# Optimization experiments

Hardware: AMD Instinct MI355X
Metric: run time of the kernel (lower is better)

## Reference

```python
import jax, jax.numpy as jnp
import numpy as np

LATENT_NUM = 64
N_FEATURES = 10000
BATCH = 4096


def setup_inputs() -> dict:
    key = jax.random.key(0)
    k1, k2 = jax.random.split(key)
    inputs = jax.random.normal(k1, (BATCH, N_FEATURES), dtype=jnp.float32)
    # TruncatedNormal(mean=0, stddev=0.01) approximated with clipped normal
    embedding = jnp.clip(
        jax.random.normal(k2, (N_FEATURES, LATENT_NUM), dtype=jnp.float32) * 0.01,
        -0.02, 0.02,
    )
    return {"inputs": inputs, "embedding": embedding}


def reference(inputs, embedding):
    # Original TF code, per latent dim f:
    #   ex2 = (sum over batch AND features of V[:,f]*X)^2   (reduce_sum w/o axis)
    # Vectorized: t[f] = sum_b (X @ V)[b,f];  q[f] = sum_{b} (X^2 @ V^2)[b,f]
    xv = inputs @ embedding                      # [B, F]
    t = jnp.sum(xv, axis=0)                      # [F]
    q = jnp.sum((inputs * inputs) @ (embedding * embedding), axis=(0, 1))  # scalar
    return 0.5 * (jnp.sum(t * t) - q)
```

## Files before the change

### kernel.cpp

```cpp
#include <hip/hip_runtime.h>

#define NROWS 4096
#define NCOLS 10000
#define NLAT  64
#define NCOLG 2500
#define TPB   256
#define NBX   10
#define NRC   128
#define RPC   32
#define NCB   40
#define CPB   250
#define NSLICE 16
#define CPS   (NRC / NSLICE)
#define NBLK2 (NCB * NSLICE)

__global__ __launch_bounds__(TPB) void colsum_partials(
        const float* __restrict__ X,
        float* __restrict__ ps, float* __restrict__ ps2) {
    int jg = blockIdx.x * TPB + threadIdx.x;
    if (jg >= NCOLG) return;
    const float* p = X + (size_t)blockIdx.y * RPC * NCOLS + (size_t)jg * 4;
    float s0=0.f,s1=0.f,s2=0.f,s3=0.f,q0=0.f,q1=0.f,q2=0.f,q3=0.f;
    #pragma unroll 8
    for (int r = 0; r < RPC; ++r) {
        float4 v = *reinterpret_cast<const float4*>(p);
        p += NCOLS;
        s0 += v.x; s1 += v.y; s2 += v.z; s3 += v.w;
        q0 = fmaf(v.x, v.x, q0); q1 = fmaf(v.y, v.y, q1);
        q2 = fmaf(v.z, v.z, q2); q3 = fmaf(v.w, v.w, q3);
    }
    size_t o = (size_t)blockIdx.y * NCOLS + (size_t)jg * 4;
    *reinterpret_cast<float4*>(ps  + o) = make_float4(s0, s1, s2, s3);
    *reinterpret_cast<float4*>(ps2 + o) = make_float4(q0, q1, q2, q3);
}

__global__ __launch_bounds__(TPB) void fold_qt(
        const float* __restrict__ ps, const float* __restrict__ ps2,
        const float* __restrict__ V, float* __restrict__ tpT) {
    const int cb = blockIdx.x;
    const int sl = blockIdx.y;
    const int tid = threadIdx.x;
    __shared__ float lds_s[CPB], lds_s2[CPB];
    if (tid < CPB) {
        const int col = cb * CPB + tid;
        float s = 0.f, s2 = 0.f;
        const int c0 = sl * CPS;
        #pragma unroll
        for (int c = c0; c < c0 + CPS; ++c) {
            s  += ps [(size_t)c * NCOLS + col];
            s2 += ps2[(size_t)c * NCOLS + col];
        }
        lds_s[tid] = s; lds_s2[tid] = s2;
    }
    __syncthreads();

    const int lane = tid & 63, w = tid >> 6;
    float at = 0.f, aq = 0.f;
    const float* Vb = V + (size_t)cb * CPB * NLAT;
    #pragma unroll 4
    for (int c = w; c < CPB; c += 4) {
        float v = Vb[(size_t)c * NLAT + lane];
        at = fmaf(lds_s[c], v, at);
        aq = fmaf(lds_s2[c], v * v, aq);
    }
    #pragma unroll
    for (int st = 1; st < 64; st <<= 1) aq += __shfl_xor(aq, st, 64);

    __shared__ float lt[4][NLAT];
    __shared__ float lq[4];
    lt[w][lane] = at;
    if (lane == 0) lq[w] = aq;
    __syncthreads();

    const int bid = sl * NCB + cb;
    if (tid < NLAT)
        tpT[(size_t)tid * NBLK2 + bid] = lt[0][tid] + lt[1][tid]
                                       + lt[2][tid] + lt[3][tid];
    if (tid == 0)
        tpT[(size_t)NLAT * NBLK2 + bid] = lq[0] + lq[1] + lq[2] + lq[3];
}

__global__ __launch_bounds__(1024) void finalize(
        const float* __restrict__ tpT, float* __restrict__ out) {
    const int tid = threadIdx.x, lane = tid & 63, w = tid >> 6;
    __shared__ float red[NLAT + 1];
    for (int r = w; r < NLAT + 1; r += 16) {
        const float* row = tpT + (size_t)r * NBLK2;
        float a = 0.f;
        #pragma unroll
        for (int i = 0; i < NBLK2 / 64; ++i) a += row[i * 64 + lane];
        #pragma unroll
        for (int st = 1; st < 64; st <<= 1) a += __shfl_xor(a, st, 64);
        if (lane == 0) red[r] = a;
    }
    __syncthreads();
    if (w == 0) {
        float t = red[lane];
        float d = t * t;
        #pragma unroll
        for (int st = 1; st < 64; st <<= 1) d += __shfl_xor(d, st, 64);
        if (lane == 0) out[0] = 0.5f * (d - red[NLAT]);
    }
}

extern "C" void kernel_launch(void* const* d_in, const int* in_sizes, int n_in,
                              void* d_out, int out_size, void* d_ws, size_t ws_size,
                              hipStream_t stream) {
    const float* X = (const float*)d_in[0];
    const float* V = (const float*)d_in[1];
    float* out = (float*)d_out;

    float* ps  = (float*)d_ws;
    float* ps2 = ps  + (size_t)NRC * NCOLS;
    float* tpT = ps2 + (size_t)NRC * NCOLS;

    colsum_partials<<<dim3(NBX, NRC), TPB, 0, stream>>>(X, ps, ps2);
    fold_qt<<<dim3(NCB, NSLICE), TPB, 0, stream>>>(ps, ps2, V, tpT);
    finalize<<<1, 1024, 0, stream>>>(tpT, out);
}
```

Baseline: 42.88 us.

## Repartition column-sum kernel into 2000-column blocks with two float4 slots per thread

The first kernel now splits columns into 5 blocks of 2000, each thread covering up to two float4 columns, and splits rows into 256 chunks of 16 instead of 128 chunks of 32. This removes idle threads in the last column block and gives each thread two independent loads per row, while the finer row split creates more blocks. The cost is twice as much partial-sum data written and read by the fold kernel, which now uses 32 slices.

```diff
diff --git a/kernel.cpp b/kernel.cpp
--- a/kernel.cpp
+++ b/kernel.cpp
@@ -3,35 +3,45 @@
 #define NROWS 4096
 #define NCOLS 10000
 #define NLAT  64
-#define NCOLG 2500
 #define TPB   256
-#define NBX   10
-#define NRC   128
-#define RPC   32
+#define NBX   5
+#define COLB  2000
+#define SLOT2 (COLB / 4 - 256)
+#define NRC   256
+#define RPC   16
 #define NCB   40
 #define CPB   250
-#define NSLICE 16
+#define NSLICE 32
 #define CPS   (NRC / NSLICE)
 #define NBLK2 (NCB * NSLICE)
 
 __global__ __launch_bounds__(TPB) void colsum_partials(
         const float* __restrict__ X,
         float* __restrict__ ps, float* __restrict__ ps2) {
-    int jg = blockIdx.x * TPB + threadIdx.x;
-    if (jg >= NCOLG) return;
-    const float* p = X + (size_t)blockIdx.y * RPC * NCOLS + (size_t)jg * 4;
-    float s0=0.f,s1=0.f,s2=0.f,s3=0.f,q0=0.f,q1=0.f,q2=0.f,q3=0.f;
-    #pragma unroll 8
+    const int bx = blockIdx.x, by = blockIdx.y, t = threadIdx.x;
+    const float* rowp = X + (size_t)by * RPC * NCOLS + (size_t)bx * COLB;
+    float4 s0 = make_float4(0.f, 0.f, 0.f, 0.f), s1 = s0, q0 = s0, q1 = s0;
+    #pragma unroll 4
     for (int r = 0; r < RPC; ++r) {
-        float4 v = *reinterpret_cast<const float4*>(p);
-        p += NCOLS;
-        s0 += v.x; s1 += v.y; s2 += v.z; s3 += v.w;
-        q0 = fmaf(v.x, v.x, q0); q1 = fmaf(v.y, v.y, q1);
-        q2 = fmaf(v.z, v.z, q2); q3 = fmaf(v.w, v.w, q3);
+        float4 a = *reinterpret_cast<const float4*>(rowp + (size_t)t * 4);
+        s0.x += a.x; s0.y += a.y; s0.z += a.z; s0.w += a.w;
+        q0.x = fmaf(a.x, a.x, q0.x); q0.y = fmaf(a.y, a.y, q0.y);
+        q0.z = fmaf(a.z, a.z, q0.z); q0.w = fmaf(a.w, a.w, q0.w);
+        if (t < SLOT2) {
+            float4 b = *reinterpret_cast<const float4*>(rowp + (size_t)(256 + t) * 4);
+            s1.x += b.x; s1.y += b.y; s1.z += b.z; s1.w += b.w;
+            q1.x = fmaf(b.x, b.x, q1.x); q1.y = fmaf(b.y, b.y, q1.y);
+            q1.z = fmaf(b.z, b.z, q1.z); q1.w = fmaf(b.w, b.w, q1.w);
+        }
+        rowp += NCOLS;
     }
-    size_t o = (size_t)blockIdx.y * NCOLS + (size_t)jg * 4;
-    *reinterpret_cast<float4*>(ps  + o) = make_float4(s0, s1, s2, s3);
-    *reinterpret_cast<float4*>(ps2 + o) = make_float4(q0, q1, q2, q3);
+    size_t o = (size_t)by * NCOLS + (size_t)bx * COLB;
+    *reinterpret_cast<float4*>(ps  + o + (size_t)t * 4) = s0;
+    *reinterpret_cast<float4*>(ps2 + o + (size_t)t * 4) = q0;
+    if (t < SLOT2) {
+        *reinterpret_cast<float4*>(ps  + o + (size_t)(256 + t) * 4) = s1;
+        *reinterpret_cast<float4*>(ps2 + o + (size_t)(256 + t) * 4) = q1;
+    }
 }
 
 __global__ __launch_bounds__(TPB) void fold_qt(
```

Result: slower. 48.26 us (+12.5%).
